# Optimization experiments

Measured on AMD Instinct MI355X. Metric: run time of the kernel, lower is better.

The kernel has to match this reference:

```python
import jax, jax.numpy as jnp
import numpy as np

B, N, E_PER = 1000, 100, 1000   # graphs, nodes per graph, edges per graph
F_IN, H = 14, 128
K1, K2 = 80, 64                 # ceil(0.8*100), ceil(0.8*80)
BN = B * N
E = B * E_PER


def setup_inputs() -> dict:
    key = jax.random.key(0)
    ks = jax.random.split(key, 12)
    x = jax.random.normal(ks[0], (BN, F_IN), jnp.float32)
    # intra-graph random edges, offset to global node ids
    intra = jax.random.randint(ks[1], (2, E), 0, N, dtype=jnp.int32)
    offs = jnp.repeat(jnp.arange(B, dtype=jnp.int32) * N, E_PER)
    edge_index = intra + offs[None, :]

    def w(k, shape):
        return 0.05 * jax.random.normal(k, shape, jnp.float32)

    return {
        "x": x,
        "edge_index": edge_index,
        "W_rel1": w(ks[2], (F_IN, H)), "W_root1": w(ks[3], (F_IN, H)), "b1": jnp.zeros((H,), jnp.float32),
        "p1": w(ks[4], (H,)),
        "W_rel2": w(ks[5], (H, H)), "W_root2": w(ks[6], (H, H)), "b2": jnp.zeros((H,), jnp.float32),
        "p2": w(ks[7], (H,)),
        "l1w": w(ks[8], (2 * H, H)), "l1b": jnp.zeros((H,), jnp.float32),
        "l2w": w(ks[9], (H, 32)), "l2b": jnp.zeros((32,), jnp.float32),
        "l3w": w(ks[10], (32, 2)), "l3b": jnp.zeros((2,), jnp.float32),
    }


def _graph_conv(x, src, dst, W_rel, W_root, b, edge_mask=None):
    # PyG GraphConv (aggr='add'): lin_rel(sum_j x_j) + lin_root(x) + bias
    msg = x[src]                      # [E, H] gather
    if edge_mask is not None:
        msg = msg * edge_mask[:, None]
    agg = jax.ops.segment_sum(msg, dst, num_segments=BN)  # scatter-add
    return agg @ W_rel + x @ W_root + b


def _topk_pool(x, w, alive, k):
    # PyG TopKPooling: score = tanh(x.w/||w||); keep top-k per graph; x *= score
    s = jnp.tanh((x @ w) / jnp.linalg.norm(w))          # [BN]
    s_m = jnp.where(alive > 0, s, -jnp.inf).reshape(B, N)
    _, idx = jax.lax.top_k(s_m, k)                      # [B, k]
    mask = jnp.zeros((B, N), x.dtype).at[jnp.arange(B)[:, None], idx].set(1.0).reshape(BN)
    return x * (s * mask)[:, None], mask


def _readout(x, mask, k):
    # cat(global_mean_pool, global_max_pool); dead nodes are already zeroed in x
    xg = x.reshape(B, N, H)
    mean = xg.sum(axis=1) / k
    mx = jnp.where(mask.reshape(B, N, 1) > 0, xg, -jnp.inf).max(axis=1)
    return jnp.concatenate([mean, mx], axis=-1)          # [B, 2H]


def reference(x, edge_index, W_rel1, W_root1, b1, p1, W_rel2, W_root2, b2, p2,
              l1w, l1b, l2w, l2b, l3w, l3b):
    src, dst = edge_index[0], edge_index[1]
    h = jax.nn.relu(_graph_conv(x, src, dst, W_rel1, W_root1, b1))
    h, m1 = _topk_pool(h, p1, jnp.ones((BN,), h.dtype), K1)
    x1 = _readout(h, m1, K1)
    em = m1[src] * m1[dst]           # edges surviving pool1
    h = jax.nn.relu(_graph_conv(h, src, dst, W_rel2, W_root2, b2, em))
    h, m2 = _topk_pool(h, p2, m1, K2)
    x2 = _readout(h, m2, K2)
    z = x1 + x2
    z = jax.nn.relu(z @ l1w + l1b)
    z = jax.nn.relu(z @ l2w + l2b)   # dropout = identity in eval mode
    return jax.nn.log_softmax(z @ l3w + l3b, axis=-1)
```

## Files before the change

kernel.cpp:

```cpp
#include <hip/hip_runtime.h>
#include <math.h>

#define NB 1000
#define NN 100
#define EPG 1000
#define FIN 14
#define HD 128
#define KP1 80
#define KP2 64
#define NT 512

#define O_HS   0
#define O_CB   12800
#define O_WL   25600
#define O_SS   33792
#define O_RP   34792
#define O_SC   34896
#define O_MK1  34996
#define O_MK2  35096
#define O_P1   35196
#define O_P2   35324
#define O_ZSH  35452
#define O_ZRD  35708
#define O_INV  36220
#define NSM    36222
#define SMEM_BYTES (NSM * 4)

__global__ __launch_bounds__(NT, 2) void fused_gnn(
    const float* __restrict__ x, const int* __restrict__ ei,
    const float* __restrict__ Wrel1, const float* __restrict__ Wroot1,
    const float* __restrict__ b1, const float* __restrict__ p1,
    const float* __restrict__ Wrel2, const float* __restrict__ Wroot2,
    const float* __restrict__ b2, const float* __restrict__ p2,
    const float* __restrict__ l1w, const float* __restrict__ l1b,
    const float* __restrict__ l2w, const float* __restrict__ l2b,
    const float* __restrict__ l3w, const float* __restrict__ l3b,
    float* __restrict__ out)
{
    extern __shared__ float smf[];
    float* Hs  = smf + O_HS;
    float* CB  = smf + O_CB;
    float* Wl  = smf + O_WL;
    float* xg  = CB;
    float* ag  = CB + 1600;
    int*   ssrc = (int*)(smf + O_SS);
    int*   rowptr = (int*)(smf + O_RP);
    float* sc  = smf + O_SC;
    float* mk1 = smf + O_MK1;
    float* mk2 = smf + O_MK2;
    float* p1s = smf + O_P1;
    float* p2s = smf + O_P2;
    float* zsh = smf + O_ZSH;
    float* zrd = smf + O_ZRD;
    int*   zdi = (int*)(smf + O_ZRD);
    float* inv = smf + O_INV;

    const int tid = threadIdx.x;
    const int g = blockIdx.x;
    const int bn = g * NN;
    const int* srcp = ei + g * EPG;
    const int* dstp = ei + NB * EPG + g * EPG;

    for (int t = tid; t < 1600; t += NT) {
        int i = t >> 4, f = t & 15;
        xg[t] = (f < FIN) ? x[bn * FIN + i * FIN + f] : 0.f;
        ag[t] = 0.f;
    }
    if (tid < 128) { p1s[tid] = p1[tid]; p2s[tid] = p2[tid]; zdi[tid] = 0; }
    if (tid >= 256 && tid < 320) {
        int l = tid - 256;
        float a = p1[l], b = p1[l + 64];
        float v = a * a + b * b;
        for (int s = 1; s < 64; s <<= 1) v += __shfl_xor(v, s);
        if (l == 0) inv[0] = rsqrtf(v);
    } else if (tid >= 320 && tid < 384) {
        int l = tid - 320;
        float a = p2[l], b = p2[l + 64];
        float v = a * a + b * b;
        for (int s = 1; s < 64; s <<= 1) v += __shfl_xor(v, s);
        if (l == 0) inv[1] = rsqrtf(v);
    }
    __syncthreads();

    for (int e = tid; e < EPG; e += NT) {
        int dl = dstp[e] - bn;
        atomicAdd(&zdi[dl], 1);
    }
    __syncthreads();
    if (tid < 64) {
        int a = zdi[tid], b = zdi[tid + 64];
        for (int off = 1; off < 64; off <<= 1) { int t = __shfl_up(a, off); if (tid >= off) a += t; }
        int totA = __shfl(a, 63);
        for (int off = 1; off < 64; off <<= 1) { int t = __shfl_up(b, off); if (tid >= off) b += t; }
        b += totA;
        rowptr[tid + 1] = a;
        if (tid + 65 <= 103) rowptr[tid + 65] = b;
        if (tid == 0) rowptr[0] = 0;
    }
    __syncthreads();
    if (tid < NN) zdi[128 + tid] = rowptr[tid];
    __syncthreads();
    for (int e = tid; e < EPG; e += NT) {
        int sl = srcp[e] - bn;
        int dl = dstp[e] - bn;
        int slot = atomicAdd(&zdi[128 + dl], 1);
        ssrc[slot] = sl;
    }
    __syncthreads();

    {
        const int f = tid & 15;
        if (f < FIN) {
            for (int i = tid >> 4; i < NN; i += 32) {
                int s0 = rowptr[i], s1 = rowptr[i + 1];
                float s = 0.f;
                for (int sl0 = s0; sl0 < s1; ++sl0)
                    s += xg[ssrc[sl0] * 16 + f];
                ag[i * 16 + f] = s;
            }
        }
    }
    __syncthreads();

    {
        const int j = tid & 127;
        float wr[FIN], wo[FIN];
#pragma unroll
        for (int k = 0; k < FIN; ++k) { wr[k] = Wrel1[k * HD + j]; wo[k] = Wroot1[k * HD + j]; }
        const float bb = b1[j];
        for (int i = tid >> 7; i < NN; i += 4) {
            float s = bb;
#pragma unroll
            for (int k = 0; k < FIN; ++k)
                s += ag[i * 16 + k] * wr[k] + xg[i * 16 + k] * wo[k];
            Hs[i * HD + j] = fmaxf(s, 0.f);
        }
    }
    __syncthreads();

    if (tid < 400) {
        const int row = tid >> 2, q = tid & 3;
        float d = 0.f;
        for (int kk = 0; kk < 32; ++kk) {
            int k = q * 32 + ((kk + tid) & 31);
            d += Hs[row * HD + k] * p1s[k];
        }
        d += __shfl_xor(d, 1);
        d += __shfl_xor(d, 2);
        if (q == 0) sc[row] = tanhf(d * inv[0]);
    }
    __syncthreads();
    if (tid < 400) {
        const int row = tid >> 2, q = tid & 3;
        float si = sc[row]; int cnt = 0;
        for (int j2 = q * 25; j2 < q * 25 + 25; ++j2) cnt += (sc[j2] > si) ? 1 : 0;
        cnt += __shfl_xor(cnt, 1);
        cnt += __shfl_xor(cnt, 2);
        if (q == 0) mk1[row] = (cnt < KP1) ? 1.f : 0.f;
    }
    __syncthreads();
    for (int o = tid; o < NN * HD; o += NT) { int i = o >> 7; Hs[o] *= sc[i] * mk1[i]; }
    __syncthreads();
    {
        const int col = tid & 127, ch = tid >> 7;
        float mean = 0.f, mx = -1e30f;
        for (int i = ch * 25; i < ch * 25 + 25; ++i) {
            float v = Hs[i * HD + col];
            mean += v;
            if (mk1[i] > 0.f && v > mx) mx = v;
        }
        zrd[tid] = mean; CB[tid] = mx;
    }
    __syncthreads();
    if (tid < HD) {
        float mean = zrd[tid] + zrd[128 + tid] + zrd[256 + tid] + zrd[384 + tid];
        float mx = fmaxf(fmaxf(CB[tid], CB[128 + tid]), fmaxf(CB[256 + tid], CB[384 + tid]));
        zsh[tid] = mean * (1.f / KP1);
        zsh[HD + tid] = mx;
    }

    const int tr = tid >> 5, tc = tid & 31;
    const int i0 = tr * 7, j0 = tc * 4;

    int rowc[7];
#pragma unroll
    for (int r = 0; r < 7; ++r) rowc[r] = (i0 + r < NN) ? (i0 + r) : (NN - 1);

    float acc[7][4];
    {
        float4 bv = ((const float4*)b2)[tc];
#pragma unroll
        for (int r = 0; r < 7; ++r) { acc[r][0] = bv.x; acc[r][1] = bv.y; acc[r][2] = bv.z; acc[r][3] = bv.w; }
    }

#define STAGE_W(SRC, HALF)                                                  \
    for (int t = tid; t < 2048; t += NT)                                    \
        ((float4*)Wl)[t] = ((const float4*)(SRC))[(HALF) * 2048 + t];

#define CONV2_FMA_HALF(ABASE, KOFF)                                         \
    for (int k0 = 0; k0 < 64; k0 += 4) {                                    \
        const float* wl = Wl + k0 * HD + j0;                                \
        float4 w0 = *(const float4*)(wl);                                   \
        float4 w1 = *(const float4*)(wl + HD);                              \
        float4 w2 = *(const float4*)(wl + 2 * HD);                          \
        float4 w3 = *(const float4*)(wl + 3 * HD);                          \
        _Pragma("unroll")                                                   \
        for (int r = 0; r < 7; ++r) {                                       \
            float4 a = *(const float4*)&ABASE[rowc[r] * HD + (KOFF) + k0];  \
            acc[r][0] += a.x * w0.x + a.y * w1.x + a.z * w2.x + a.w * w3.x; \
            acc[r][1] += a.x * w0.y + a.y * w1.y + a.z * w2.y + a.w * w3.y; \
            acc[r][2] += a.x * w0.z + a.y * w1.z + a.z * w2.z + a.w * w3.z; \
            acc[r][3] += a.x * w0.w + a.y * w1.w + a.z * w2.w + a.w * w3.w; \
        }                                                                   \
    }

    STAGE_W(Wroot2, 0);
    __syncthreads();
    CONV2_FMA_HALF(Hs, 0)
    __syncthreads();
    STAGE_W(Wroot2, 1);
    __syncthreads();
    CONV2_FMA_HALF(Hs, 64)
    __syncthreads();

    for (int t = tid; t < NN * 32; t += NT) {
        int i = t >> 5, jj = t & 31;
        int s0 = rowptr[i], s1 = rowptr[i + 1];
        float4 s = {0.f, 0.f, 0.f, 0.f};
        for (int e = s0; e < s1; ++e) {
            const float4 v = *(const float4*)&Hs[ssrc[e] * HD + 4 * jj];
            s.x += v.x; s.y += v.y; s.z += v.z; s.w += v.w;
        }
        *(float4*)&CB[i * HD + 4 * jj] = s;
    }
    STAGE_W(Wrel2, 0);
    __syncthreads();
    CONV2_FMA_HALF(CB, 0)
    __syncthreads();
    STAGE_W(Wrel2, 1);
    __syncthreads();
    CONV2_FMA_HALF(CB, 64)
    __syncthreads();

#pragma unroll
    for (int r = 0; r < 7; ++r) {
        if (i0 + r < NN) {
            float4 v;
            v.x = fmaxf(acc[r][0], 0.f); v.y = fmaxf(acc[r][1], 0.f);
            v.z = fmaxf(acc[r][2], 0.f); v.w = fmaxf(acc[r][3], 0.f);
            *(float4*)&Hs[(i0 + r) * HD + j0] = v;
        }
    }
    __syncthreads();

    if (tid < 400) {
        const int row = tid >> 2, q = tid & 3;
        float d = 0.f;
        for (int kk = 0; kk < 32; ++kk) {
            int k = q * 32 + ((kk + tid) & 31);
            d += Hs[row * HD + k] * p2s[k];
        }
        d += __shfl_xor(d, 1);
        d += __shfl_xor(d, 2);
        if (q == 0) sc[row] = (mk1[row] > 0.f) ? tanhf(d * inv[1]) : -1e30f;
    }
    __syncthreads();
    if (tid < 400) {
        const int row = tid >> 2, q = tid & 3;
        float si = sc[row]; int cnt = 0;
        for (int j2 = q * 25; j2 < q * 25 + 25; ++j2) cnt += (sc[j2] > si) ? 1 : 0;
        cnt += __shfl_xor(cnt, 1);
        cnt += __shfl_xor(cnt, 2);
        if (q == 0) mk2[row] = (mk1[row] > 0.f && cnt < KP2) ? 1.f : 0.f;
    }
    __syncthreads();
    for (int o = tid; o < NN * HD; o += NT) { int i = o >> 7; Hs[o] *= sc[i] * mk2[i]; }
    __syncthreads();
    {
        const int col = tid & 127, ch = tid >> 7;
        float mean = 0.f, mx = -1e30f;
        for (int i = ch * 25; i < ch * 25 + 25; ++i) {
            float v = Hs[i * HD + col];
            mean += v;
            if (mk2[i] > 0.f && v > mx) mx = v;
        }
        zrd[tid] = mean; CB[tid] = mx;
    }
    __syncthreads();
    if (tid < HD) {
        float mean = zrd[tid] + zrd[128 + tid] + zrd[256 + tid] + zrd[384 + tid];
        float mx = fmaxf(fmaxf(CB[tid], CB[128 + tid]), fmaxf(CB[256 + tid], CB[384 + tid]));
        zsh[tid] += mean * (1.f / KP2);
        zsh[HD + tid] += mx;
    }
    __syncthreads();

    {
        const int j = tid & 127, q = tid >> 7;
        float a = 0.f;
        for (int kk = 0; kk < 64; ++kk) {
            int k = q * 64 + kk;
            a += zsh[k] * l1w[k * HD + j];
        }
        zrd[tid] = a;
    }
    __syncthreads();
    if (tid < HD)
        CB[tid] = fmaxf(zrd[tid] + zrd[128 + tid] + zrd[256 + tid] + zrd[384 + tid] + l1b[tid], 0.f);
    __syncthreads();
    if (tid < 256) {
        const int o = tid & 31, q = tid >> 5;
        float a = 0.f;
        for (int kk = 0; kk < 16; ++kk) {
            int k = q * 16 + kk;
            a += CB[k] * l2w[k * 32 + o];
        }
        zrd[tid] = a;
    }
    __syncthreads();
    if (tid < 32) {
        float v = l2b[tid];
#pragma unroll
        for (int q = 0; q < 8; ++q) v += zrd[q * 32 + tid];
        CB[256 + tid] = fmaxf(v, 0.f);
    }
    __syncthreads();
    if (tid == 0) {
        float o0 = l3b[0], o1 = l3b[1];
        for (int k = 0; k < 32; ++k) {
            float v = CB[256 + k];
            o0 += v * l3w[2 * k];
            o1 += v * l3w[2 * k + 1];
        }
        float m = fmaxf(o0, o1);
        float l = m + logf(expf(o0 - m) + expf(o1 - m));
        out[g * 2 + 0] = o0 - l;
        out[g * 2 + 1] = o1 - l;
    }
}

extern "C" void kernel_launch(void* const* d_in, const int* in_sizes, int n_in,
                              void* d_out, int out_size, void* d_ws, size_t ws_size,
                              hipStream_t stream)
{
    const float* x      = (const float*)d_in[0];
    const int*   ei     = (const int*)d_in[1];
    const float* Wrel1  = (const float*)d_in[2];
    const float* Wroot1 = (const float*)d_in[3];
    const float* b1     = (const float*)d_in[4];
    const float* p1     = (const float*)d_in[5];
    const float* Wrel2  = (const float*)d_in[6];
    const float* Wroot2 = (const float*)d_in[7];
    const float* b2     = (const float*)d_in[8];
    const float* p2     = (const float*)d_in[9];
    const float* l1w    = (const float*)d_in[10];
    const float* l1b    = (const float*)d_in[11];
    const float* l2w    = (const float*)d_in[12];
    const float* l2b    = (const float*)d_in[13];
    const float* l3w    = (const float*)d_in[14];
    const float* l3b    = (const float*)d_in[15];
    float* out = (float*)d_out;

    (void)hipFuncSetAttribute((const void*)fused_gnn,
                              hipFuncAttributeMaxDynamicSharedMemorySize, SMEM_BYTES);

    fused_gnn<<<dim3(NB), dim3(NT), SMEM_BYTES, stream>>>(
        x, ei, Wrel1, Wroot1, b1, p1, Wrel2, Wroot2, b2, p2,
        l1w, l1b, l2w, l2b, l3w, l3b, out);
}
```

Measured before the change: 284.8 us.

## Shrink LDS footprint via chunked conv2 aggregation, 16-row weight slices, ushort edges

Cuts the shared-memory footprint to roughly 80KB per block. Conv2 weights are now staged in 16-row slices with register prefetch of the next slice instead of 64-row halves. The neighbour aggregation for conv2 is done in four 32-column chunks, so the aggregate buffer only needs 100x32 floats. Edge source indices are stored as 16-bit values. The aim is to let more blocks fit per CU, or at least hide global weight-load latency through the prefetch. The price is many more __syncthreads barriers and repeated rowptr/edge walks, once per chunk.

```diff
diff --git a/kernel.cpp b/kernel.cpp
--- a/kernel.cpp
+++ b/kernel.cpp
@@ -12,18 +12,18 @@
 
 #define O_HS   0
 #define O_CB   12800
-#define O_WL   25600
-#define O_SS   33792
-#define O_RP   34792
-#define O_SC   34896
-#define O_MK1  34996
-#define O_MK2  35096
-#define O_P1   35196
-#define O_P2   35324
-#define O_ZSH  35452
-#define O_ZRD  35708
-#define O_INV  36220
-#define NSM    36222
+#define O_WL   16000
+#define O_SS   18048
+#define O_RP   18548
+#define O_SC   18652
+#define O_MK1  18752
+#define O_MK2  18852
+#define O_P1   18952
+#define O_P2   19080
+#define O_ZSH  19208
+#define O_ZRD  19464
+#define O_INV  19976
+#define NSM    19978
 #define SMEM_BYTES (NSM * 4)
 
 __global__ __launch_bounds__(NT, 2) void fused_gnn(
@@ -43,7 +43,7 @@
     float* Wl  = smf + O_WL;
     float* xg  = CB;
     float* ag  = CB + 1600;
-    int*   ssrc = (int*)(smf + O_SS);
+    unsigned short* ssrc = (unsigned short*)(smf + O_SS);
     int*   rowptr = (int*)(smf + O_RP);
     float* sc  = smf + O_SC;
     float* mk1 = smf + O_MK1;
@@ -104,7 +104,7 @@
         int sl = srcp[e] - bn;
         int dl = dstp[e] - bn;
         int slot = atomicAdd(&zdi[128 + dl], 1);
-        ssrc[slot] = sl;
+        ssrc[slot] = (unsigned short)sl;
     }
     __syncthreads();
 
@@ -115,7 +115,7 @@
                 int s0 = rowptr[i], s1 = rowptr[i + 1];
                 float s = 0.f;
                 for (int sl0 = s0; sl0 < s1; ++sl0)
-                    s += xg[ssrc[sl0] * 16 + f];
+                    s += xg[(int)ssrc[sl0] * 16 + f];
                 ag[i * 16 + f] = s;
             }
         }
@@ -193,12 +193,11 @@
         for (int r = 0; r < 7; ++r) { acc[r][0] = bv.x; acc[r][1] = bv.y; acc[r][2] = bv.z; acc[r][3] = bv.w; }
     }
 
-#define STAGE_W(SRC, HALF)                                                  \
-    for (int t = tid; t < 2048; t += NT)                                    \
-        ((float4*)Wl)[t] = ((const float4*)(SRC))[(HALF) * 2048 + t];
-
-#define CONV2_FMA_HALF(ABASE, KOFF)                                         \
-    for (int k0 = 0; k0 < 64; k0 += 4) {                                    \
+    const float4* Wroot2v = (const float4*)Wroot2;
+    const float4* Wrel2v  = (const float4*)Wrel2;
+
+#define FMA_SLICE(ABASE, LD, KOFF)                                          \
+    for (int k0 = 0; k0 < 16; k0 += 4) {                                    \
         const float* wl = Wl + k0 * HD + j0;                                \
         float4 w0 = *(const float4*)(wl);                                   \
         float4 w1 = *(const float4*)(wl + HD);                              \
@@ -206,7 +205,7 @@
         float4 w3 = *(const float4*)(wl + 3 * HD);                          \
         _Pragma("unroll")                                                   \
         for (int r = 0; r < 7; ++r) {                                       \
-            float4 a = *(const float4*)&ABASE[rowc[r] * HD + (KOFF) + k0];  \
+            float4 a = *(const float4*)&ABASE[rowc[r] * (LD) + (KOFF) + k0];\
             acc[r][0] += a.x * w0.x + a.y * w1.x + a.z * w2.x + a.w * w3.x; \
             acc[r][1] += a.x * w0.y + a.y * w1.y + a.z * w2.y + a.w * w3.y; \
             acc[r][2] += a.x * w0.z + a.y * w1.z + a.z * w2.z + a.w * w3.z; \
@@ -214,32 +213,37 @@
         }                                                                   \
     }
 
-    STAGE_W(Wroot2, 0);
-    __syncthreads();
-    CONV2_FMA_HALF(Hs, 0)
-    __syncthreads();
-    STAGE_W(Wroot2, 1);
-    __syncthreads();
-    CONV2_FMA_HALF(Hs, 64)
-    __syncthreads();
-
-    for (int t = tid; t < NN * 32; t += NT) {
-        int i = t >> 5, jj = t & 31;
-        int s0 = rowptr[i], s1 = rowptr[i + 1];
-        float4 s = {0.f, 0.f, 0.f, 0.f};
-        for (int e = s0; e < s1; ++e) {
-            const float4 v = *(const float4*)&Hs[ssrc[e] * HD + 4 * jj];
-            s.x += v.x; s.y += v.y; s.z += v.z; s.w += v.w;
-        }
-        *(float4*)&CB[i * HD + 4 * jj] = s;
-    }
-    STAGE_W(Wrel2, 0);
-    __syncthreads();
-    CONV2_FMA_HALF(CB, 0)
-    __syncthreads();
-    STAGE_W(Wrel2, 1);
-    __syncthreads();
-    CONV2_FMA_HALF(CB, 64)
+    float4 pre = Wroot2v[tid];
+    for (int s = 0; s < 8; ++s) {
+        __syncthreads();
+        ((float4*)Wl)[tid] = pre;
+        pre = (s < 7) ? Wroot2v[(s + 1) * 512 + tid]
+                      : Wrel2v[tid];
+        __syncthreads();
+        FMA_SLICE(Hs, HD, s * 16)
+    }
+
+    for (int c = 0; c < 4; ++c) {
+        __syncthreads();
+        for (int t = tid; t < 800; t += NT) {
+            int i = t >> 3, jj = t & 7;
+            int s0 = rowptr[i], s1 = rowptr[i + 1];
+            float4 s = {0.f, 0.f, 0.f, 0.f};
+            for (int e = s0; e < s1; ++e) {
+                const float4 v = *(const float4*)&Hs[(int)ssrc[e] * HD + c * 32 + jj * 4];
+                s.x += v.x; s.y += v.y; s.z += v.z; s.w += v.w;
+            }
+            *(float4*)&CB[i * 32 + jj * 4] = s;
+        }
+        for (int s2 = 0; s2 < 2; ++s2) {
+            __syncthreads();
+            ((float4*)Wl)[tid] = pre;
+            int nxt = c * 2 + s2 + 1;
+            if (nxt < 8) pre = Wrel2v[nxt * 512 + tid];
+            __syncthreads();
+            FMA_SLICE(CB, 32, s2 * 16)
+        }
+    }
     __syncthreads();
 
 #pragma unroll
```

Measured after the change: 279.9 us. About the same (-1.7%).
